# Optimization experiments

Hardware: AMD Instinct MI355X
Metric: run time of the kernel (lower is better)

## Reference

```python
import jax, jax.numpy as jnp
import numpy as np

INF = 1e9  # large finite sentinel (avoid inf arithmetic in potentials)


def _hungarian(cost):
    """Exact linear sum assignment (Jonker-Volgenant style shortest augmenting
    path, O(N^3)) on a single [N, N] cost matrix. Returns col_ind (int32 [N])
    such that row i is matched to column col_ind[i] with minimal total cost
    (same solution as scipy.optimize.linear_sum_assignment up to ties).
    Column index n is a virtual 'start' column (e-maxx formulation)."""
    n = cost.shape[0]

    def row_body(i, carry):
        u, v, p = carry  # u: row potentials [n]; v: col potentials [n+1]; p[j]: row assigned to col j (-1 free)
        p = p.at[n].set(i)
        state = (u, v, p,
                 jnp.full(n + 1, INF, cost.dtype),   # minv
                 jnp.zeros(n + 1, dtype=bool),       # used
                 jnp.zeros(n + 1, dtype=jnp.int32),  # way (parent col on path)
                 jnp.int32(n))                       # j0 current col

        def cond(st):
            _, _, p_, _, _, _, j0 = st
            return p_[j0] >= 0  # stop when we reach a free column

        def body(st):
            u_, v_, p_, minv, used, way, j0 = st
            used = used.at[j0].set(True)
            i0 = p_[j0]
            cur = cost[i0] - u_[i0] - v_[:n]          # reduced costs of row i0 [n]
            cur = jnp.where(used[:n], INF, cur)
            better = cur < minv[:n]
            minv = minv.at[:n].set(jnp.where(better, cur, minv[:n]))
            way = way.at[:n].set(jnp.where(better, j0, way[:n]))
            masked = jnp.where(used[:n], INF, minv[:n])
            j1 = jnp.argmin(masked).astype(jnp.int32)
            delta = masked[j1]
            # dual update: used cols raise row potential, others shrink minv
            u_ = u_.at[p_].add(jnp.where(used, delta, jnp.zeros((), cost.dtype)))
            v_ = jnp.where(used, v_ - delta, v_)
            minv = jnp.where(used, minv, minv - delta)
            return (u_, v_, p_, minv, used, way, j1)

        u, v, p, _, _, way, j0 = jax.lax.while_loop(cond, body, state)

        # augment along the alternating path back to the virtual column
        def cond2(s):
            j, _ = s
            return j != n

        def body2(s):
            j, p_ = s
            j_prev = way[j]
            return j_prev, p_.at[j].set(p_[j_prev])

        _, p = jax.lax.while_loop(cond2, body2, (j0, p))
        return (u, v, p)

    u0 = jnp.zeros(n, cost.dtype)
    v0 = jnp.zeros(n + 1, cost.dtype)
    p0 = jnp.full(n + 1, -1, dtype=jnp.int32)
    _, _, p = jax.lax.fori_loop(0, n, row_body, (u0, v0, p0))
    # p[j] = row matched to col j  ->  col_ind[row] = j
    col_ind = jnp.zeros(n, jnp.int32).at[p[:n]].set(jnp.arange(n, dtype=jnp.int32))
    return col_ind


def setup_inputs() -> dict:
    key = jax.random.key(0)
    k1, k2 = jax.random.split(key)
    B, N, D = 2048, 24, 256
    slots = jax.random.normal(k1, (B, N, D), dtype=jnp.float32)
    prev_slots = jax.random.normal(k2, (B, N, D), dtype=jnp.float32)
    return {"slots": slots, "prev_slots": prev_slots}


def reference(slots, prev_slots):
    """HungarianPredictor.forward with similarity='cosine': reorder current
    slots to align with prev_slots ordering via optimal 1-1 matching."""
    eps = 1e-12  # torch F.normalize eps
    pn = prev_slots / jnp.maximum(
        jnp.linalg.norm(prev_slots, axis=-1, keepdims=True), eps)
    cn = slots / jnp.maximum(
        jnp.linalg.norm(slots, axis=-1, keepdims=True), eps)
    # cost[b, i, j] = 1 - <prev_i, curr_j>   [B, N, N]
    cost = 1.0 - jnp.einsum('bnd,bmd->bnm', pn, cn)
    col = jax.vmap(_hungarian)(jax.lax.stop_gradient(cost))  # [B, N] int32
    reordered = jax.vmap(lambda s, c: s[c])(slots, col)       # gather per batch
    return reordered
```

## Files before the change

### kernel.cpp

```cpp
#include <hip/hip_runtime.h>
#include <math.h>

#define N    24
#define D    256
#define BLK  256
#define NB   4
#define CTS  28
#define INFV 1e9f

__device__ __forceinline__ int readlane_i(int x, int l) {
    return __builtin_amdgcn_readlane(x, l);
}
__device__ __forceinline__ float readlane_f(float x, int l) {
    return __uint_as_float((unsigned)__builtin_amdgcn_readlane((int)__float_as_uint(x), l));
}

__device__ __forceinline__ unsigned wave_min32(unsigned x) {
    unsigned t;
    t = (unsigned)__builtin_amdgcn_update_dpp((int)x, (int)x, 0xB1,  0xF, 0xF, false); x = t < x ? t : x;
    t = (unsigned)__builtin_amdgcn_update_dpp((int)x, (int)x, 0x4E,  0xF, 0xF, false); x = t < x ? t : x;
    t = (unsigned)__builtin_amdgcn_update_dpp((int)x, (int)x, 0x114, 0xF, 0xF, false); x = t < x ? t : x;
    t = (unsigned)__builtin_amdgcn_update_dpp((int)x, (int)x, 0x118, 0xF, 0xF, false); x = t < x ? t : x;
    t = (unsigned)__builtin_amdgcn_update_dpp((int)x, (int)x, 0x142, 0xF, 0xF, false); x = t < x ? t : x;
    return x;
}

__device__ __forceinline__ unsigned packkey(float x, int lane) {
    unsigned key = __float_as_uint(x);
    key ^= (unsigned)((int)key >> 31) | 0x80000000u;
    return (key & 0xFFFFFFC0u) | (unsigned)lane;
}

#define DOT4(a, b) ((a).x*(b).x + (a).y*(b).y + (a).z*(b).z + (a).w*(b).w)
#define LGKM0() __asm__ volatile("s_waitcnt lgkmcnt(0)" ::: "memory")

__global__ __launch_bounds__(BLK) void hungarian_fused(
    const float* __restrict__ slots,
    const float* __restrict__ prev,
    float* __restrict__ out, int B)
{
    __shared__ __align__(16) float costT[NB][N][CTS];
    __shared__ int winner[NB][N];
    __shared__ int colw[NB][N];

    const int tid  = threadIdx.x;
    const int lane = tid & 63;
    const int wv   = tid >> 6;
    const int bw   = blockIdx.x * NB + wv;
    if (bw >= B) return;

    const int rg = lane >> 3;
    const int cg = lane & 7;
    const float4* pA = (const float4*)(prev  + (size_t)bw * N * D) + rg * 3 * (D / 4);
    const float4* pC = (const float4*)(slots + (size_t)bw * N * D) + cg * 3 * (D / 4);

    float s00=0,s01=0,s02=0,s10=0,s11=0,s12=0,s20=0,s21=0,s22=0;
    float pa0=0,pa1=0,pa2=0,pc0=0,pc1=0,pc2=0;
    #pragma unroll 4
    for (int k = 0; k < 64; ++k) {
        float4 a0 = pA[k], a1 = pA[64+k], a2 = pA[128+k];
        float4 b0 = pC[k], b1 = pC[64+k], b2 = pC[128+k];
        s00 += DOT4(a0,b0); s01 += DOT4(a0,b1); s02 += DOT4(a0,b2);
        s10 += DOT4(a1,b0); s11 += DOT4(a1,b1); s12 += DOT4(a1,b2);
        s20 += DOT4(a2,b0); s21 += DOT4(a2,b1); s22 += DOT4(a2,b2);
        pa0 += DOT4(a0,a0); pa1 += DOT4(a1,a1); pa2 += DOT4(a2,a2);
        pc0 += DOT4(b0,b0); pc1 += DOT4(b1,b1); pc2 += DOT4(b2,b2);
    }
    float ira0 = 1.0f / fmaxf(sqrtf(pa0), 1e-12f);
    float ira1 = 1.0f / fmaxf(sqrtf(pa1), 1e-12f);
    float ira2 = 1.0f / fmaxf(sqrtf(pa2), 1e-12f);
    float irc0 = 1.0f / fmaxf(sqrtf(pc0), 1e-12f);
    float irc1 = 1.0f / fmaxf(sqrtf(pc1), 1e-12f);
    float irc2 = 1.0f / fmaxf(sqrtf(pc2), 1e-12f);

    {
        float* ct = &costT[wv][0][0];
        const int cb = cg * 3, rb = rg * 3;
        ct[(cb+0)*CTS + rb+0] = 1.0f - s00*ira0*irc0;
        ct[(cb+1)*CTS + rb+0] = 1.0f - s01*ira0*irc1;
        ct[(cb+2)*CTS + rb+0] = 1.0f - s02*ira0*irc2;
        ct[(cb+0)*CTS + rb+1] = 1.0f - s10*ira1*irc0;
        ct[(cb+1)*CTS + rb+1] = 1.0f - s11*ira1*irc1;
        ct[(cb+2)*CTS + rb+1] = 1.0f - s12*ira1*irc2;
        ct[(cb+0)*CTS + rb+2] = 1.0f - s20*ira2*irc0;
        ct[(cb+1)*CTS + rb+2] = 1.0f - s21*ira2*irc1;
        ct[(cb+2)*CTS + rb+2] = 1.0f - s22*ira2*irc2;
    }
    LGKM0();

    const bool isCol = (lane < N);
    const int  jj    = isCol ? lane : 0;
    float cq[24];
    {
        const float4* cp4 = (const float4*)&costT[wv][jj][0];
        #pragma unroll
        for (int r = 0; r < 6; ++r) {
            float4 q = cp4[r];
            cq[r*4+0] = q.x; cq[r*4+1] = q.y; cq[r*4+2] = q.z; cq[r*4+3] = q.w;
        }
    }

    const int cl = (lane < N) ? lane : (N - 1);
    const float* __restrict__ ctcol = &costT[wv][cl][0];

    float cm = cq[0]; int ri = 0;
    #pragma unroll
    for (int i = 1; i < N; ++i) { if (cq[i] < cm) { cm = cq[i]; ri = i; } }

    if (isCol) winner[wv][lane] = -1;
    LGKM0();
    if (isCol) winner[wv][ri] = lane;
    LGKM0();
    int p = -1;
    if (isCol && winner[wv][ri] == lane) p = ri;
    const int widx = isCol ? lane : 0;
    unsigned long long mm = __ballot(isCol && winner[wv][widx] >= 0);
    unsigned freeRows = (~(unsigned)mm) & ((1u << N) - 1);

    float uu  = 0.0f;
    float v   = isCol ? cm : INFV;
    int   way = -1;

    while (freeRows) {
        const int f = (int)__builtin_ctz(freeRows);
        freeRows &= freeRows - 1;

        float minv  = INFV;
        bool  used  = false;
        bool  inTree = false;
        int   s_j0 = -1;
        int   s_i0 = f;
        float s_u0 = readlane_f(uu, f);
        int   j1   = 0;

        while (true) {
            inTree = inTree || (lane == s_i0);
            used   = used   || (lane == s_j0);

            float cij = ctcol[s_i0];
            float cur = cij - s_u0 - v;
            bool  act = isCol && !used;
            if (act && cur < minv) { minv = cur; way = s_j0; }
            float masked = act ? minv : INFV;

            unsigned kmin = (unsigned)readlane_i(
                (int)wave_min32(packkey(masked, lane)), 31);
            j1 = (int)(kmin & 63u);

            float delta = readlane_f(masked, j1);
            int   i0n   = readlane_i(p, j1);
            float u0n   = readlane_f(uu, i0n & 31);

            if (inTree) uu += delta;
            if (used) v -= delta;
            else if (act) minv -= delta;

            if (i0n < 0) break;
            s_j0 = j1; s_i0 = i0n; s_u0 = u0n;
        }

        int jcur = j1;
        while (true) {
            int wj   = readlane_i(way, jcur);
            int pnew = (wj < 0) ? f : readlane_i(p, wj);
            if (lane == jcur) p = pnew;
            if (wj < 0) break;
            jcur = wj;
        }
    }

    if (isCol) colw[wv][p] = lane;
    LGKM0();

    const float4* sg4 = (const float4*)(slots + (size_t)bw * N * D);
    float4*       og4 = (float4*)(out + (size_t)bw * N * D);
    #pragma unroll
    for (int i = 0; i < N; ++i) {
        int c = colw[wv][i];
        og4[i * 64 + lane] = sg4[c * 64 + lane];
    }
}

extern "C" void kernel_launch(void* const* d_in, const int* in_sizes, int n_in,
                              void* d_out, int out_size, void* d_ws, size_t ws_size,
                              hipStream_t stream) {
    const float* slots = (const float*)d_in[0];
    const float* prev  = (const float*)d_in[1];
    float* out = (float*)d_out;
    int B = in_sizes[0] / (N * D);
    int grid = (B + NB - 1) / NB;
    hungarian_fused<<<grid, BLK, 0, stream>>>(slots, prev, out, B);
}
```

Baseline: 193.8 us.

## Cache matched-row potential per column to shorten Hungarian inner-loop dependency chain

Each column lane now keeps a copy of the row potential of its matched row (pu). The next iteration's u0 therefore comes from a single readlane on j1, instead of a readlane of p followed by a dependent readlane of uu. The inner loop becomes branchless: selected columns get minv set to INF, so the separate masked value is no longer needed, and non-column lanes start out as used. The cost-matrix row stride is padded from 28 to 33 and cost rows are read as scalars, a choice aimed at LDS bank conflicts. The dot-product unroll drops from 4 to 2. The catch is extra bookkeeping: pu must be updated on every dual step and refreshed during augmentation.

```diff
diff --git a/kernel.cpp b/kernel.cpp
--- a/kernel.cpp
+++ b/kernel.cpp
@@ -5,7 +5,7 @@
 #define D    256
 #define BLK  256
 #define NB   4
-#define CTS  28
+#define CTS  33
 #define INFV 1e9f
 
 __device__ __forceinline__ int readlane_i(int x, int l) {
@@ -39,7 +39,7 @@
     const float* __restrict__ prev,
     float* __restrict__ out, int B)
 {
-    __shared__ __align__(16) float costT[NB][N][CTS];
+    __shared__ float costT[NB][N][CTS];
     __shared__ int winner[NB][N];
     __shared__ int colw[NB][N];
 
@@ -56,7 +56,7 @@
 
     float s00=0,s01=0,s02=0,s10=0,s11=0,s12=0,s20=0,s21=0,s22=0;
     float pa0=0,pa1=0,pa2=0,pc0=0,pc1=0,pc2=0;
-    #pragma unroll 4
+    #pragma unroll 2
     for (int k = 0; k < 64; ++k) {
         float4 a0 = pA[k], a1 = pA[64+k], a2 = pA[128+k];
         float4 b0 = pC[k], b1 = pC[64+k], b2 = pC[128+k];
@@ -89,20 +89,12 @@
     LGKM0();
 
     const bool isCol = (lane < N);
-    const int  jj    = isCol ? lane : 0;
-    float cq[24];
-    {
-        const float4* cp4 = (const float4*)&costT[wv][jj][0];
-        #pragma unroll
-        for (int r = 0; r < 6; ++r) {
-            float4 q = cp4[r];
-            cq[r*4+0] = q.x; cq[r*4+1] = q.y; cq[r*4+2] = q.z; cq[r*4+3] = q.w;
-        }
-    }
-
-    const int cl = (lane < N) ? lane : (N - 1);
+    const int  cl    = isCol ? lane : (N - 1);
     const float* __restrict__ ctcol = &costT[wv][cl][0];
 
+    float cq[N];
+    #pragma unroll
+    for (int i = 0; i < N; ++i) cq[i] = ctcol[i];
     float cm = cq[0]; int ri = 0;
     #pragma unroll
     for (int i = 1; i < N; ++i) { if (cq[i] < cm) { cm = cq[i]; ri = i; } }
@@ -118,6 +110,7 @@
     unsigned freeRows = (~(unsigned)mm) & ((1u << N) - 1);
 
     float uu  = 0.0f;
+    float pu  = 0.0f;
     float v   = isCol ? cm : INFV;
     int   way = -1;
 
@@ -126,7 +119,7 @@
         freeRows &= freeRows - 1;
 
         float minv  = INFV;
-        bool  used  = false;
+        bool  used  = !isCol;
         bool  inTree = false;
         int   s_j0 = -1;
         int   s_i0 = f;
@@ -135,25 +128,30 @@
 
         while (true) {
             inTree = inTree || (lane == s_i0);
-            used   = used   || (lane == s_j0);
 
             float cij = ctcol[s_i0];
-            float cur = cij - s_u0 - v;
-            bool  act = isCol && !used;
-            if (act && cur < minv) { minv = cur; way = s_j0; }
-            float masked = act ? minv : INFV;
+            float cur = (cij - s_u0) - v;
+
+            bool imp = (!used) && (cur < minv);
+            minv = imp ? cur : minv;
+            way  = imp ? s_j0 : way;
 
             unsigned kmin = (unsigned)readlane_i(
-                (int)wave_min32(packkey(masked, lane)), 31);
+                (int)wave_min32(packkey(minv, lane)), 31);
             j1 = (int)(kmin & 63u);
 
-            float delta = readlane_f(masked, j1);
+            float delta = readlane_f(minv, j1);
             int   i0n   = readlane_i(p, j1);
-            float u0n   = readlane_f(uu, i0n & 31);
+            float u0n   = readlane_f(pu, j1);
 
-            if (inTree) uu += delta;
-            if (used) v -= delta;
-            else if (act) minv -= delta;
+            uu   = inTree ? uu + delta : uu;
+            v    = used   ? v - delta  : v;
+            pu   = used   ? pu + delta : pu;
+            minv = used   ? minv       : minv - delta;
+
+            bool sel = (lane == j1);
+            minv = sel ? INFV : minv;
+            used = used || sel;
 
             if (i0n < 0) break;
             s_j0 = j1; s_i0 = i0n; s_u0 = u0n;
@@ -161,9 +159,10 @@
 
         int jcur = j1;
         while (true) {
-            int wj   = readlane_i(way, jcur);
-            int pnew = (wj < 0) ? f : readlane_i(p, wj);
-            if (lane == jcur) p = pnew;
+            int   wj   = readlane_i(way, jcur);
+            int   pnew = (wj < 0) ? f : readlane_i(p, wj);
+            float pun  = readlane_f(uu, pnew);
+            if (lane == jcur) { p = pnew; pu = pun; }
             if (wj < 0) break;
             jcur = wj;
         }
```

Result: faster. 183.7 us (-5.2%).
